# Optimization experiments

Measured on AMD Instinct MI355X. Metric: run time of the kernel, lower is better.

The kernel has to match this reference:

```python
import jax, jax.numpy as jnp
import numpy as np

N, F_IN, E = 50000, 128, 800000
HID, HEADS, EMB = 32, 8, 64
NEG_SLOPE = 0.2


def gat_conv(x, src, dst, W_src, W_dst, att_src, att_dst, bias, heads, out_ch, concat):
    n = x.shape[0]
    h_src = (x @ W_src).reshape(n, heads, out_ch)   # [N,H,C]
    h_dst = (x @ W_dst).reshape(n, heads, out_ch)
    a_src = jnp.sum(h_src * att_src, axis=-1)       # [N,H]
    a_dst = jnp.sum(h_dst * att_dst, axis=-1)
    e = jax.nn.leaky_relu(a_src[src] + a_dst[dst], NEG_SLOPE)  # [E,H]
    # segment softmax over destination nodes (stable, max detached as in PyG)
    m = jax.ops.segment_max(e, dst, num_segments=n)
    m = jnp.where(jnp.isfinite(m), m, 0.0)
    ex = jnp.exp(e - jax.lax.stop_gradient(m)[dst])
    denom = jax.ops.segment_sum(ex, dst, num_segments=n)
    alpha = ex / (denom[dst] + 1e-16)               # [E,H]
    msg = h_src[src] * alpha[:, :, None]            # [E,H,C]
    out = jax.ops.segment_sum(msg, dst, num_segments=n)  # [N,H,C]
    if concat:
        out = out.reshape(n, heads * out_ch)
    else:
        out = out.mean(axis=1)
    return out + bias


def setup_inputs() -> dict:
    key = jax.random.key(0)
    ks = jax.random.split(key, 12)
    g = lambda k, shape: jax.random.normal(k, shape, dtype=jnp.float32) * (1.0 / np.sqrt(shape[0]))
    x = jax.random.normal(ks[0], (N, F_IN), dtype=jnp.float32)
    edge_index = jax.random.randint(ks[1], (2, E), 0, N, dtype=jnp.int64)
    return {
        "x": x,
        "edge_index": edge_index,
        "W_src1": g(ks[2], (F_IN, HEADS * HID)),
        "W_dst1": g(ks[3], (F_IN, HEADS * HID)),
        "att_src1": g(ks[4], (HEADS, HID)) * 0.1,
        "att_dst1": g(ks[5], (HEADS, HID)) * 0.1,
        "b1": jnp.zeros((HEADS * HID,), dtype=jnp.float32),
        "W_src2": g(ks[6], (HEADS * HID, EMB)),
        "W_dst2": g(ks[7], (HEADS * HID, EMB)),
        "att_src2": g(ks[8], (1, EMB)) * 0.1,
        "att_dst2": g(ks[9], (1, EMB)) * 0.1,
        "b2": jnp.zeros((EMB,), dtype=jnp.float32),
    }


def reference(x, edge_index, W_src1, W_dst1, att_src1, att_dst1, b1,
              W_src2, W_dst2, att_src2, att_dst2, b2):
    src, dst = edge_index[0], edge_index[1]
    h = gat_conv(x, src, dst, W_src1, W_dst1, att_src1, att_dst1, b1, HEADS, HID, True)
    h = jax.nn.relu(h)
    out = gat_conv(h, src, dst, W_src2, W_dst2, att_src2, att_dst2, b2, 1, EMB, False)
    return out
```

## Files before the change

kernel.cpp:

```cpp
#include <hip/hip_runtime.h>
#include <hip/hip_bf16.h>
#include <cstdint>
#include <cstddef>

#define NN    50000
#define FIN   128
#define EE    800000
#define HID_  32
#define HEADS_ 8
#define EMB_  64
#define NEG   0.2f
#define CAP   64
#define NB_PREP 202
#define NB_EDGE 3125
#define LOG2E 1.4426950408889634f

typedef short bf16x8 __attribute__((ext_vector_type(8)));
typedef float f32x4  __attribute__((ext_vector_type(4)));

static __device__ __forceinline__ ushort f2bf(float f){
    uint u = __float_as_uint(f);
    uint r = (u + 0x7FFFu + ((u >> 16) & 1u)) >> 16;
    return (ushort)r;
}
static __device__ __forceinline__ float bf2f(ushort u){
    return __uint_as_float(((uint)u) << 16);
}
static __device__ __forceinline__ float pexp(float t){
    return __builtin_amdgcn_exp2f(fmaxf(t, NEG * t));
}

__global__ __launch_bounds__(256) void k_prep_hist(const float* __restrict__ Wsrc1, const float* __restrict__ Wdst1,
                                                   const float* __restrict__ asrc1, const float* __restrict__ adst1,
                                                   const float* __restrict__ Wsrc2, const float* __restrict__ Wdst2,
                                                   const float* __restrict__ asrc2, const float* __restrict__ adst2,
                                                   ushort* __restrict__ wt1bf, float* __restrict__ wt2,
                                                   ushort* __restrict__ w1t, ushort* __restrict__ w2t,
                                                   const int* __restrict__ src, const int* __restrict__ dst,
                                                   int* __restrict__ deg, int* __restrict__ col){
    if (blockIdx.x >= NB_PREP){
        int e = (blockIdx.x - NB_PREP) * 256 + threadIdx.x;
        if (e < EE){
            int d = dst[e];
            int r = atomicAdd(&deg[d], 1);
            col[d * CAP + r] = src[e];
        }
        return;
    }
    int idx = blockIdx.x * blockDim.x + threadIdx.x;
    if (idx < 2048){
        int f = idx >> 4, j = idx & 15;
        const float* W; const float* a; int h;
        if (j < 8) { W = Wsrc1; a = asrc1; h = j; } else { W = Wdst1; a = adst1; h = j - 8; }
        float s = 0.f;
        #pragma unroll
        for (int c = 0; c < HID_; ++c)
            s += W[(size_t)f * (HEADS_ * HID_) + h * HID_ + c] * a[h * HID_ + c];
        wt1bf[j * 128 + f] = f2bf(s * LOG2E);
    } else if (idx < 2560){
        int t = idx - 2048;
        int f = t >> 1, j = t & 1;
        const float* W = j ? Wdst2 : Wsrc2;
        const float* a = j ? adst2 : asrc2;
        float s = 0.f;
        #pragma unroll
        for (int c = 0; c < EMB_; ++c) s += W[(size_t)f * EMB_ + c] * a[c];
        wt2[j * 256 + f] = s * LOG2E;
    } else if (idx < 35328){
        int t = idx - 2560;
        int n = t >> 7, k = t & 127;
        w1t[t] = f2bf(Wsrc1[(size_t)k * 256 + n]);
    } else if (idx < 51712){
        int t = idx - 35328;
        int n = t >> 8, k = t & 255;
        w2t[t] = f2bf(Wsrc2[(size_t)k * 64 + n]);
    }
}

__global__ __launch_bounds__(256) void k_gemm1_mfma(const float* __restrict__ x,
                                                    const ushort* __restrict__ w1t,
                                                    const ushort* __restrict__ wt1bf,
                                                    ushort* __restrict__ c,
                                                    float* __restrict__ a_src1,
                                                    float* __restrict__ a_dst1){
    __shared__ ushort As[64][136];
    __shared__ ushort Bs[128][136];
    __shared__ ushort Bsa[16][136];
    const int tid = threadIdx.x;
    const int m0 = blockIdx.x * 64;
    const int n0 = blockIdx.y * 128;
    #pragma unroll
    for (int i = 0; i < 8; ++i){
        int idx = tid + i * 256;
        int r = idx >> 5, c4 = idx & 31;
        int m = m0 + r;
        float4 v = make_float4(0.f, 0.f, 0.f, 0.f);
        if (m < NN) v = *(const float4*)&x[(size_t)m * FIN + c4 * 4];
        ushort4 u; u.x = f2bf(v.x); u.y = f2bf(v.y); u.z = f2bf(v.z); u.w = f2bf(v.w);
        *(ushort4*)&As[r][c4 * 4] = u;
    }
    #pragma unroll
    for (int i = 0; i < 8; ++i){
        int idx = tid + i * 256;
        int r = idx >> 4, c8 = idx & 15;
        const ushort4* s4 = (const ushort4*)&w1t[(size_t)(n0 + r) * 128 + c8 * 8];
        *(ushort4*)&Bs[r][c8 * 8]     = s4[0];
        *(ushort4*)&Bs[r][c8 * 8 + 4] = s4[1];
    }
    if (blockIdx.y == 0){
        int r = tid >> 4, c8 = tid & 15;
        const ushort4* s4 = (const ushort4*)&wt1bf[r * 128 + c8 * 8];
        *(ushort4*)&Bsa[r][c8 * 8]     = s4[0];
        *(ushort4*)&Bsa[r][c8 * 8 + 4] = s4[1];
    }
    __syncthreads();
    const int lane = tid & 63;
    const int w    = tid >> 6;
    const int mr   = lane & 15;
    const int kg   = lane >> 4;
    f32x4 acc[8];
    #pragma unroll
    for (int i = 0; i < 8; ++i) acc[i] = (f32x4){0.f, 0.f, 0.f, 0.f};
    f32x4 acca = (f32x4){0.f, 0.f, 0.f, 0.f};
    #pragma unroll
    for (int ks = 0; ks < 4; ++ks){
        bf16x8 a = *(const bf16x8*)&As[w * 16 + mr][ks * 32 + kg * 8];
        #pragma unroll
        for (int nf = 0; nf < 8; ++nf){
            bf16x8 b = *(const bf16x8*)&Bs[nf * 16 + mr][ks * 32 + kg * 8];
            acc[nf] = __builtin_amdgcn_mfma_f32_16x16x32_bf16(a, b, acc[nf], 0, 0, 0);
        }
        if (blockIdx.y == 0){
            bf16x8 ba = *(const bf16x8*)&Bsa[mr][ks * 32 + kg * 8];
            acca = __builtin_amdgcn_mfma_f32_16x16x32_bf16(a, ba, acca, 0, 0, 0);
        }
    }
    #pragma unroll
    for (int nf = 0; nf < 8; ++nf){
        int colb = n0 + nf * 16 + mr;
        #pragma unroll
        for (int r = 0; r < 4; ++r){
            int row = m0 + w * 16 + kg * 4 + r;
            if (row < NN) c[(size_t)row * 256 + colb] = f2bf(acc[nf][r]);
        }
    }
    if (blockIdx.y == 0){
        int j = mr;
        #pragma unroll
        for (int r = 0; r < 4; ++r){
            int row = m0 + w * 16 + kg * 4 + r;
            if (row < NN){
                if (j < 8) a_src1[(size_t)row * 8 + j]       = acca[r];
                else       a_dst1[(size_t)row * 8 + (j - 8)] = acca[r];
            }
        }
    }
}

__global__ __launch_bounds__(256) void k_agg1(const ushort* __restrict__ hsrc, const float* __restrict__ a_src,
                                              const float* __restrict__ a_dst, const int* __restrict__ deg,
                                              const int* __restrict__ col, const float* __restrict__ b1,
                                              const float* __restrict__ wt2,
                                              ushort* __restrict__ hout_bf,
                                              float* __restrict__ a_src2, float* __restrict__ a_dst2){
    int node = blockIdx.x * 4 + (threadIdx.x >> 6);
    if (node >= NN) return;
    int lane = threadIdx.x & 63;
    int head = lane >> 3;
    float ad = a_dst[(size_t)node * 8 + head];
    const ushort4* h4 = (const ushort4*)hsrc;
    float4 acc = make_float4(0.f, 0.f, 0.f, 0.f);
    float den = 0.f;
    int b = node * CAP, en = b + deg[node];
    int i = b;
    for (; i + 4 <= en; i += 4){
        int s0 = col[i], s1 = col[i+1], s2 = col[i+2], s3 = col[i+3];
        float e0 = a_src[(size_t)s0 * 8 + head];
        float e1 = a_src[(size_t)s1 * 8 + head];
        float e2 = a_src[(size_t)s2 * 8 + head];
        float e3 = a_src[(size_t)s3 * 8 + head];
        ushort4 v0 = h4[(size_t)s0 * 64 + lane];
        ushort4 v1 = h4[(size_t)s1 * 64 + lane];
        ushort4 v2 = h4[(size_t)s2 * 64 + lane];
        ushort4 v3 = h4[(size_t)s3 * 64 + lane];
        float p0 = pexp(e0 + ad);
        float p1 = pexp(e1 + ad);
        float p2 = pexp(e2 + ad);
        float p3 = pexp(e3 + ad);
        acc.x += p0*bf2f(v0.x) + p1*bf2f(v1.x) + p2*bf2f(v2.x) + p3*bf2f(v3.x);
        acc.y += p0*bf2f(v0.y) + p1*bf2f(v1.y) + p2*bf2f(v2.y) + p3*bf2f(v3.y);
        acc.z += p0*bf2f(v0.z) + p1*bf2f(v1.z) + p2*bf2f(v2.z) + p3*bf2f(v3.z);
        acc.w += p0*bf2f(v0.w) + p1*bf2f(v1.w) + p2*bf2f(v2.w) + p3*bf2f(v3.w);
        den += p0 + p1 + p2 + p3;
    }
    for (; i < en; ++i){
        int s = col[i];
        float p = pexp(a_src[(size_t)s * 8 + head] + ad);
        ushort4 v = h4[(size_t)s * 64 + lane];
        acc.x += p * bf2f(v.x); acc.y += p * bf2f(v.y);
        acc.z += p * bf2f(v.z); acc.w += p * bf2f(v.w);
        den += p;
    }
    float inv = 1.f / (den + 1e-16f);
    float4 bb = ((const float4*)b1)[lane];
    float4 o;
    o.x = fmaxf(acc.x * inv + bb.x, 0.f);
    o.y = fmaxf(acc.y * inv + bb.y, 0.f);
    o.z = fmaxf(acc.z * inv + bb.z, 0.f);
    o.w = fmaxf(acc.w * inv + bb.w, 0.f);
    ushort4 ob; ob.x = f2bf(o.x); ob.y = f2bf(o.y); ob.z = f2bf(o.z); ob.w = f2bf(o.w);
    ((ushort4*)hout_bf)[(size_t)node * 64 + lane] = ob;
    float4 ws4 = ((const float4*)wt2)[lane];
    float4 wd4 = ((const float4*)(wt2 + 256))[lane];
    float ss2 = o.x*ws4.x + o.y*ws4.y + o.z*ws4.z + o.w*ws4.w;
    float sd2 = o.x*wd4.x + o.y*wd4.y + o.z*wd4.z + o.w*wd4.w;
    #pragma unroll
    for (int off = 32; off > 0; off >>= 1){
        ss2 += __shfl_xor(ss2, off);
        sd2 += __shfl_xor(sd2, off);
    }
    if (lane == 0){ a_src2[node] = ss2; a_dst2[node] = sd2; }
}

__global__ __launch_bounds__(256) void k_gemm2_mfma(const ushort* __restrict__ hbf,
                                                    const ushort* __restrict__ w2t,
                                                    ushort* __restrict__ c2){
    __shared__ ushort As[64][264];
    __shared__ ushort Bs[64][264];
    const int tid = threadIdx.x;
    const int m0 = blockIdx.x * 64;
    #pragma unroll
    for (int i = 0; i < 8; ++i){
        int idx = tid + i * 256;
        int r = idx >> 5, c8 = idx & 31;
        int m = m0 + r;
        ushort4 v0 = make_ushort4(0,0,0,0), v1 = make_ushort4(0,0,0,0);
        if (m < NN){
            const ushort4* s4 = (const ushort4*)&hbf[(size_t)m * 256 + c8 * 8];
            v0 = s4[0]; v1 = s4[1];
        }
        *(ushort4*)&As[r][c8 * 8]     = v0;
        *(ushort4*)&As[r][c8 * 8 + 4] = v1;
    }
    #pragma unroll
    for (int i = 0; i < 8; ++i){
        int idx = tid + i * 256;
        int r = idx >> 5, c8 = idx & 31;
        const ushort4* s4 = (const ushort4*)&w2t[(size_t)r * 256 + c8 * 8];
        *(ushort4*)&Bs[r][c8 * 8]     = s4[0];
        *(ushort4*)&Bs[r][c8 * 8 + 4] = s4[1];
    }
    __syncthreads();
    const int lane = tid & 63;
    const int w    = tid >> 6;
    const int mr   = lane & 15;
    const int kg   = lane >> 4;
    f32x4 acc[4];
    #pragma unroll
    for (int i = 0; i < 4; ++i) acc[i] = (f32x4){0.f, 0.f, 0.f, 0.f};
    #pragma unroll
    for (int ks = 0; ks < 8; ++ks){
        bf16x8 a = *(const bf16x8*)&As[w * 16 + mr][ks * 32 + kg * 8];
        #pragma unroll
        for (int nf = 0; nf < 4; ++nf){
            bf16x8 b = *(const bf16x8*)&Bs[nf * 16 + mr][ks * 32 + kg * 8];
            acc[nf] = __builtin_amdgcn_mfma_f32_16x16x32_bf16(a, b, acc[nf], 0, 0, 0);
        }
    }
    #pragma unroll
    for (int nf = 0; nf < 4; ++nf){
        int colb = nf * 16 + mr;
        #pragma unroll
        for (int r = 0; r < 4; ++r){
            int row = m0 + w * 16 + kg * 4 + r;
            if (row < NN) c2[(size_t)row * 64 + colb] = f2bf(acc[nf][r]);
        }
    }
}

__global__ __launch_bounds__(256) void k_agg2(const ushort* __restrict__ h2bf, const float* __restrict__ a_src2,
                                              const float* __restrict__ a_dst2, const int* __restrict__ deg,
                                              const int* __restrict__ col, const float* __restrict__ b2,
                                              float* __restrict__ out){
    int node = blockIdx.x * 4 + (threadIdx.x >> 6);
    if (node >= NN) return;
    int lane = threadIdx.x & 63;
    float ad = a_dst2[node];
    float acc = 0.f, den = 0.f;
    int b = node * CAP, en = b + deg[node];
    int i = b;
    for (; i + 8 <= en; i += 8){
        int ss[8]; float e[8]; ushort u[8]; float p[8];
        #pragma unroll
        for (int j = 0; j < 8; ++j) ss[j] = col[i + j];
        #pragma unroll
        for (int j = 0; j < 8; ++j) e[j] = a_src2[ss[j]];
        #pragma unroll
        for (int j = 0; j < 8; ++j) u[j] = h2bf[(size_t)ss[j] * 64 + lane];
        #pragma unroll
        for (int j = 0; j < 8; ++j) p[j] = pexp(e[j] + ad);
        #pragma unroll
        for (int j = 0; j < 8; ++j){
            acc += p[j] * bf2f(u[j]);
            den += p[j];
        }
    }
    for (; i < en; ++i){
        int s = col[i];
        float p = pexp(a_src2[s] + ad);
        acc += p * bf2f(h2bf[(size_t)s * 64 + lane]);
        den += p;
    }
    out[(size_t)node * 64 + lane] = acc / (den + 1e-16f) + b2[lane];
}

extern "C" void kernel_launch(void* const* d_in, const int* in_sizes, int n_in,
                              void* d_out, int out_size, void* d_ws, size_t ws_size,
                              hipStream_t stream){
    const float* x        = (const float*)d_in[0];
    const int*   ei       = (const int*)  d_in[1];
    const float* Wsrc1    = (const float*)d_in[2];
    const float* Wdst1    = (const float*)d_in[3];
    const float* att_src1 = (const float*)d_in[4];
    const float* att_dst1 = (const float*)d_in[5];
    const float* b1       = (const float*)d_in[6];
    const float* Wsrc2    = (const float*)d_in[7];
    const float* Wdst2    = (const float*)d_in[8];
    const float* att_src2 = (const float*)d_in[9];
    const float* att_dst2 = (const float*)d_in[10];
    const float* b2       = (const float*)d_in[11];
    float* out = (float*)d_out;
    const int* srcp = ei;
    const int* dstp = ei + EE;

    char* base = (char*)d_ws;
    ushort* hbf1   = (ushort*)base;  base += (size_t)NN * 256 * 2;
    ushort* hrel   = (ushort*)base;  base += (size_t)NN * 256 * 2;
    ushort* h2bf   = (ushort*)base;  base += (size_t)NN * 64 * 2;
    float*  a_src1 = (float*)base;   base += (size_t)NN * 8 * 4;
    float*  a_dst1 = (float*)base;   base += (size_t)NN * 8 * 4;
    float*  a_src2 = (float*)base;   base += (size_t)NN * 4;
    float*  a_dst2 = (float*)base;   base += (size_t)NN * 4;
    ushort* wt1bf  = (ushort*)base;  base += 2048 * 2;
    float*  wt2    = (float*)base;   base += 512 * 4;
    ushort* w1t    = (ushort*)base;  base += 32768 * 2;
    ushort* w2t    = (ushort*)base;  base += 16384 * 2;
    int* deg     = (int*)base;       base += (size_t)NN * 4;
    int* col     = (int*)base;       base += (size_t)NN * CAP * 4;

    (void)hipMemsetAsync(deg, 0, NN * sizeof(int), stream);

    k_prep_hist<<<NB_PREP + NB_EDGE, 256, 0, stream>>>(Wsrc1, Wdst1, att_src1, att_dst1,
                                                       Wsrc2, Wdst2, att_src2, att_dst2,
                                                       wt1bf, wt2, w1t, w2t,
                                                       srcp, dstp, deg, col);
    dim3 g1((NN + 63) / 64, 2);
    k_gemm1_mfma<<<g1, 256, 0, stream>>>(x, w1t, wt1bf, hbf1, a_src1, a_dst1);
    k_agg1<<<(NN + 3) / 4, 256, 0, stream>>>(hbf1, a_src1, a_dst1, deg, col, b1, wt2,
                                             hrel, a_src2, a_dst2);
    k_gemm2_mfma<<<(NN + 63) / 64, 256, 0, stream>>>(hrel, w2t, h2bf);
    k_agg2<<<(NN + 3) / 4, 256, 0, stream>>>(h2bf, a_src2, a_dst2, deg, col, b2, out);
}
```

Baseline: 208.4 us.

## Fuse edge bucketing into GEMM1 launch and drop LDS staging in both GEMMs

Moves the edge histogram/bucketing work out of the weight-prep kernel into the first GEMM launch as extra blocks, so the atomic scatter runs alongside the projection GEMM instead of before it. GEMM1 now computes all 256 output columns per block in a 1D grid, so x is read once rather than twice. Both GEMMs drop shared-memory staging and load A and B fragments straight from global memory into MFMA operands, removing syncthreads and LDS traffic. In exchange, each GEMM1 block holds 16 accumulator tiles, which raises register pressure, and B fragments are re-read from global/L2 by every wave.

```diff
diff --git a/kernel.cpp b/kernel.cpp
--- a/kernel.cpp
+++ b/kernel.cpp
@@ -13,6 +13,7 @@
 #define CAP   64
 #define NB_PREP 202
 #define NB_EDGE 3125
+#define NB_M1   782
 #define LOG2E 1.4426950408889634f
 
 typedef short bf16x8 __attribute__((ext_vector_type(8)));
@@ -30,23 +31,12 @@
     return __builtin_amdgcn_exp2f(fmaxf(t, NEG * t));
 }
 
-__global__ __launch_bounds__(256) void k_prep_hist(const float* __restrict__ Wsrc1, const float* __restrict__ Wdst1,
-                                                   const float* __restrict__ asrc1, const float* __restrict__ adst1,
-                                                   const float* __restrict__ Wsrc2, const float* __restrict__ Wdst2,
-                                                   const float* __restrict__ asrc2, const float* __restrict__ adst2,
-                                                   ushort* __restrict__ wt1bf, float* __restrict__ wt2,
-                                                   ushort* __restrict__ w1t, ushort* __restrict__ w2t,
-                                                   const int* __restrict__ src, const int* __restrict__ dst,
-                                                   int* __restrict__ deg, int* __restrict__ col){
-    if (blockIdx.x >= NB_PREP){
-        int e = (blockIdx.x - NB_PREP) * 256 + threadIdx.x;
-        if (e < EE){
-            int d = dst[e];
-            int r = atomicAdd(&deg[d], 1);
-            col[d * CAP + r] = src[e];
-        }
-        return;
-    }
+__global__ __launch_bounds__(256) void k_prep(const float* __restrict__ Wsrc1, const float* __restrict__ Wdst1,
+                                              const float* __restrict__ asrc1, const float* __restrict__ adst1,
+                                              const float* __restrict__ Wsrc2, const float* __restrict__ Wdst2,
+                                              const float* __restrict__ asrc2, const float* __restrict__ adst2,
+                                              ushort* __restrict__ wt1bf, float* __restrict__ wt2,
+                                              ushort* __restrict__ w1t, ushort* __restrict__ w2t){
     int idx = blockIdx.x * blockDim.x + threadIdx.x;
     if (idx < 2048){
         int f = idx >> 4, j = idx & 15;
@@ -77,74 +67,65 @@
     }
 }
 
-__global__ __launch_bounds__(256) void k_gemm1_mfma(const float* __restrict__ x,
-                                                    const ushort* __restrict__ w1t,
-                                                    const ushort* __restrict__ wt1bf,
-                                                    ushort* __restrict__ c,
-                                                    float* __restrict__ a_src1,
-                                                    float* __restrict__ a_dst1){
-    __shared__ ushort As[64][136];
-    __shared__ ushort Bs[128][136];
-    __shared__ ushort Bsa[16][136];
-    const int tid = threadIdx.x;
-    const int m0 = blockIdx.x * 64;
-    const int n0 = blockIdx.y * 128;
-    #pragma unroll
-    for (int i = 0; i < 8; ++i){
-        int idx = tid + i * 256;
-        int r = idx >> 5, c4 = idx & 31;
-        int m = m0 + r;
-        float4 v = make_float4(0.f, 0.f, 0.f, 0.f);
-        if (m < NN) v = *(const float4*)&x[(size_t)m * FIN + c4 * 4];
-        ushort4 u; u.x = f2bf(v.x); u.y = f2bf(v.y); u.z = f2bf(v.z); u.w = f2bf(v.w);
-        *(ushort4*)&As[r][c4 * 4] = u;
-    }
-    #pragma unroll
-    for (int i = 0; i < 8; ++i){
-        int idx = tid + i * 256;
-        int r = idx >> 4, c8 = idx & 15;
-        const ushort4* s4 = (const ushort4*)&w1t[(size_t)(n0 + r) * 128 + c8 * 8];
-        *(ushort4*)&Bs[r][c8 * 8]     = s4[0];
-        *(ushort4*)&Bs[r][c8 * 8 + 4] = s4[1];
-    }
-    if (blockIdx.y == 0){
-        int r = tid >> 4, c8 = tid & 15;
-        const ushort4* s4 = (const ushort4*)&wt1bf[r * 128 + c8 * 8];
-        *(ushort4*)&Bsa[r][c8 * 8]     = s4[0];
-        *(ushort4*)&Bsa[r][c8 * 8 + 4] = s4[1];
-    }
-    __syncthreads();
+__global__ __launch_bounds__(256) void k_gemm1_bucket(const float* __restrict__ x,
+                                                      const ushort* __restrict__ w1t,
+                                                      const ushort* __restrict__ wt1bf,
+                                                      ushort* __restrict__ c,
+                                                      float* __restrict__ a_src1,
+                                                      float* __restrict__ a_dst1,
+                                                      const int* __restrict__ src, const int* __restrict__ dst,
+                                                      int* __restrict__ deg, int* __restrict__ col){
+    if (blockIdx.x >= NB_M1){
+        int e = (blockIdx.x - NB_M1) * 256 + threadIdx.x;
+        if (e < EE){
+            int d = dst[e];
+            int r = atomicAdd(&deg[d], 1);
+            col[d * CAP + r] = src[e];
+        }
+        return;
+    }
+    const int tid  = threadIdx.x;
     const int lane = tid & 63;
     const int w    = tid >> 6;
     const int mr   = lane & 15;
     const int kg   = lane >> 4;
-    f32x4 acc[8];
-    #pragma unroll
-    for (int i = 0; i < 8; ++i) acc[i] = (f32x4){0.f, 0.f, 0.f, 0.f};
+    const int m0   = blockIdx.x * 64;
+    const int arow = m0 + w * 16 + mr;
+    const bool rv  = arow < NN;
+    f32x4 acc[16];
+    #pragma unroll
+    for (int i = 0; i < 16; ++i) acc[i] = (f32x4){0.f, 0.f, 0.f, 0.f};
     f32x4 acca = (f32x4){0.f, 0.f, 0.f, 0.f};
     #pragma unroll
     for (int ks = 0; ks < 4; ++ks){
-        bf16x8 a = *(const bf16x8*)&As[w * 16 + mr][ks * 32 + kg * 8];
-        #pragma unroll
-        for (int nf = 0; nf < 8; ++nf){
-            bf16x8 b = *(const bf16x8*)&Bs[nf * 16 + mr][ks * 32 + kg * 8];
+        bf16x8 a = (bf16x8){0,0,0,0,0,0,0,0};
+        if (rv){
+            const float* ap = &x[(size_t)arow * FIN + ks * 32 + kg * 8];
+            float4 f0 = *(const float4*)ap;
+            float4 f1 = *(const float4*)(ap + 4);
+            a[0] = (short)f2bf(f0.x); a[1] = (short)f2bf(f0.y);
+            a[2] = (short)f2bf(f0.z); a[3] = (short)f2bf(f0.w);
+            a[4] = (short)f2bf(f1.x); a[5] = (short)f2bf(f1.y);
+            a[6] = (short)f2bf(f1.z); a[7] = (short)f2bf(f1.w);
+        }
+        #pragma unroll
+        for (int nf = 0; nf < 16; ++nf){
+            bf16x8 b = *(const bf16x8*)&w1t[(size_t)(nf * 16 + mr) * 128 + ks * 32 + kg * 8];
             acc[nf] = __builtin_amdgcn_mfma_f32_16x16x32_bf16(a, b, acc[nf], 0, 0, 0);
         }
-        if (blockIdx.y == 0){
-            bf16x8 ba = *(const bf16x8*)&Bsa[mr][ks * 32 + kg * 8];
-            acca = __builtin_amdgcn_mfma_f32_16x16x32_bf16(a, ba, acca, 0, 0, 0);
-        }
-    }
-    #pragma unroll
-    for (int nf = 0; nf < 8; ++nf){
-        int colb = n0 + nf * 16 + mr;
+        bf16x8 ba = *(const bf16x8*)&wt1bf[mr * 128 + ks * 32 + kg * 8];
+        acca = __builtin_amdgcn_mfma_f32_16x16x32_bf16(a, ba, acca, 0, 0, 0);
+    }
+    #pragma unroll
+    for (int nf = 0; nf < 16; ++nf){
+        int colb = nf * 16 + mr;
         #pragma unroll
         for (int r = 0; r < 4; ++r){
             int row = m0 + w * 16 + kg * 4 + r;
             if (row < NN) c[(size_t)row * 256 + colb] = f2bf(acc[nf][r]);
         }
     }
-    if (blockIdx.y == 0){
+    {
         int j = mr;
         #pragma unroll
         for (int r = 0; r < 4; ++r){
@@ -222,48 +203,27 @@
     if (lane == 0){ a_src2[node] = ss2; a_dst2[node] = sd2; }
 }
 
-__global__ __launch_bounds__(256) void k_gemm2_mfma(const ushort* __restrict__ hbf,
+__global__ __launch_bounds__(256) void k_gemm2_lite(const ushort* __restrict__ hrel,
                                                     const ushort* __restrict__ w2t,
                                                     ushort* __restrict__ c2){
-    __shared__ ushort As[64][264];
-    __shared__ ushort Bs[64][264];
-    const int tid = threadIdx.x;
-    const int m0 = blockIdx.x * 64;
-    #pragma unroll
-    for (int i = 0; i < 8; ++i){
-        int idx = tid + i * 256;
-        int r = idx >> 5, c8 = idx & 31;
-        int m = m0 + r;
-        ushort4 v0 = make_ushort4(0,0,0,0), v1 = make_ushort4(0,0,0,0);
-        if (m < NN){
-            const ushort4* s4 = (const ushort4*)&hbf[(size_t)m * 256 + c8 * 8];
-            v0 = s4[0]; v1 = s4[1];
-        }
-        *(ushort4*)&As[r][c8 * 8]     = v0;
-        *(ushort4*)&As[r][c8 * 8 + 4] = v1;
-    }
-    #pragma unroll
-    for (int i = 0; i < 8; ++i){
-        int idx = tid + i * 256;
-        int r = idx >> 5, c8 = idx & 31;
-        const ushort4* s4 = (const ushort4*)&w2t[(size_t)r * 256 + c8 * 8];
-        *(ushort4*)&Bs[r][c8 * 8]     = s4[0];
-        *(ushort4*)&Bs[r][c8 * 8 + 4] = s4[1];
-    }
-    __syncthreads();
+    const int tid  = threadIdx.x;
     const int lane = tid & 63;
     const int w    = tid >> 6;
     const int mr   = lane & 15;
     const int kg   = lane >> 4;
+    const int m0   = blockIdx.x * 64;
+    const int arow = m0 + w * 16 + mr;
+    const bool rv  = arow < NN;
     f32x4 acc[4];
     #pragma unroll
     for (int i = 0; i < 4; ++i) acc[i] = (f32x4){0.f, 0.f, 0.f, 0.f};
     #pragma unroll
     for (int ks = 0; ks < 8; ++ks){
-        bf16x8 a = *(const bf16x8*)&As[w * 16 + mr][ks * 32 + kg * 8];
+        bf16x8 a = (bf16x8){0,0,0,0,0,0,0,0};
+        if (rv) a = *(const bf16x8*)&hrel[(size_t)arow * 256 + ks * 32 + kg * 8];
         #pragma unroll
         for (int nf = 0; nf < 4; ++nf){
-            bf16x8 b = *(const bf16x8*)&Bs[nf * 16 + mr][ks * 32 + kg * 8];
+            bf16x8 b = *(const bf16x8*)&w2t[(size_t)(nf * 16 + mr) * 256 + ks * 32 + kg * 8];
             acc[nf] = __builtin_amdgcn_mfma_f32_16x16x32_bf16(a, b, acc[nf], 0, 0, 0);
         }
     }
@@ -350,14 +310,13 @@
 
     (void)hipMemsetAsync(deg, 0, NN * sizeof(int), stream);
 
-    k_prep_hist<<<NB_PREP + NB_EDGE, 256, 0, stream>>>(Wsrc1, Wdst1, att_src1, att_dst1,
-                                                       Wsrc2, Wdst2, att_src2, att_dst2,
-                                                       wt1bf, wt2, w1t, w2t,
-                                                       srcp, dstp, deg, col);
-    dim3 g1((NN + 63) / 64, 2);
-    k_gemm1_mfma<<<g1, 256, 0, stream>>>(x, w1t, wt1bf, hbf1, a_src1, a_dst1);
+    k_prep<<<NB_PREP, 256, 0, stream>>>(Wsrc1, Wdst1, att_src1, att_dst1,
+                                        Wsrc2, Wdst2, att_src2, att_dst2,
+                                        wt1bf, wt2, w1t, w2t);
+    k_gemm1_bucket<<<NB_M1 + NB_EDGE, 256, 0, stream>>>(x, w1t, wt1bf, hbf1, a_src1, a_dst1,
+                                                        srcp, dstp, deg, col);
     k_agg1<<<(NN + 3) / 4, 256, 0, stream>>>(hbf1, a_src1, a_dst1, deg, col, b1, wt2,
                                              hrel, a_src2, a_dst2);
-    k_gemm2_mfma<<<(NN + 63) / 64, 256, 0, stream>>>(hrel, w2t, h2bf);
+    k_gemm2_lite<<<NB_M1, 256, 0, stream>>>(hrel, w2t, h2bf);
     k_agg2<<<(NN + 3) / 4, 256, 0, stream>>>(h2bf, a_src2, a_dst2, deg, col, b2, out);
 }
```

Result: slower. 244.1 us (+17.2%).

## Fold deg memset into prep kernel and fuse edge histogram into GEMM1 launch

Applied to the files above, without the earlier changes.

The memset of the degree array moves into the weight-prep kernel, which now covers 202 blocks × 256 = 51,712 threads, enough to zero all N entries. The edge bucketing (atomic degree count plus CSR column scatter) moves out of the prep kernel into extra blocks appended to the first GEMM grid. The 2D GEMM grid is flattened into 1D to make room for this. This removes one memset launch and lets the atomic-heavy histogram run alongside the MFMA GEMM instead of before it. In exchange, the histogram blocks share the launch with GEMM blocks that reserve large shared memory, which may limit occupancy.

```diff
diff --git a/kernel.cpp b/kernel.cpp
--- a/kernel.cpp
+++ b/kernel.cpp
@@ -13,6 +13,7 @@
 #define CAP   64
 #define NB_PREP 202
 #define NB_EDGE 3125
+#define NB_G1   1564
 #define LOG2E 1.4426950408889634f
 
 typedef short bf16x8 __attribute__((ext_vector_type(8)));
@@ -30,24 +31,15 @@
     return __builtin_amdgcn_exp2f(fmaxf(t, NEG * t));
 }
 
-__global__ __launch_bounds__(256) void k_prep_hist(const float* __restrict__ Wsrc1, const float* __restrict__ Wdst1,
-                                                   const float* __restrict__ asrc1, const float* __restrict__ adst1,
-                                                   const float* __restrict__ Wsrc2, const float* __restrict__ Wdst2,
-                                                   const float* __restrict__ asrc2, const float* __restrict__ adst2,
-                                                   ushort* __restrict__ wt1bf, float* __restrict__ wt2,
-                                                   ushort* __restrict__ w1t, ushort* __restrict__ w2t,
-                                                   const int* __restrict__ src, const int* __restrict__ dst,
-                                                   int* __restrict__ deg, int* __restrict__ col){
-    if (blockIdx.x >= NB_PREP){
-        int e = (blockIdx.x - NB_PREP) * 256 + threadIdx.x;
-        if (e < EE){
-            int d = dst[e];
-            int r = atomicAdd(&deg[d], 1);
-            col[d * CAP + r] = src[e];
-        }
-        return;
-    }
+__global__ __launch_bounds__(256) void k_prep(const float* __restrict__ Wsrc1, const float* __restrict__ Wdst1,
+                                              const float* __restrict__ asrc1, const float* __restrict__ adst1,
+                                              const float* __restrict__ Wsrc2, const float* __restrict__ Wdst2,
+                                              const float* __restrict__ asrc2, const float* __restrict__ adst2,
+                                              ushort* __restrict__ wt1bf, float* __restrict__ wt2,
+                                              ushort* __restrict__ w1t, ushort* __restrict__ w2t,
+                                              int* __restrict__ deg){
     int idx = blockIdx.x * blockDim.x + threadIdx.x;
+    if (idx < NN) deg[idx] = 0;
     if (idx < 2048){
         int f = idx >> 4, j = idx & 15;
         const float* W; const float* a; int h;
@@ -77,18 +69,29 @@
     }
 }
 
-__global__ __launch_bounds__(256) void k_gemm1_mfma(const float* __restrict__ x,
+__global__ __launch_bounds__(256) void k_gemm1_hist(const float* __restrict__ x,
                                                     const ushort* __restrict__ w1t,
                                                     const ushort* __restrict__ wt1bf,
                                                     ushort* __restrict__ c,
                                                     float* __restrict__ a_src1,
-                                                    float* __restrict__ a_dst1){
+                                                    float* __restrict__ a_dst1,
+                                                    const int* __restrict__ src, const int* __restrict__ dst,
+                                                    int* __restrict__ deg, int* __restrict__ col){
     __shared__ ushort As[64][136];
     __shared__ ushort Bs[128][136];
     __shared__ ushort Bsa[16][136];
+    if (blockIdx.x >= NB_G1){
+        int e = (blockIdx.x - NB_G1) * 256 + threadIdx.x;
+        if (e < EE){
+            int d = dst[e];
+            int r = atomicAdd(&deg[d], 1);
+            col[d * CAP + r] = src[e];
+        }
+        return;
+    }
     const int tid = threadIdx.x;
-    const int m0 = blockIdx.x * 64;
-    const int n0 = blockIdx.y * 128;
+    const int m0 = (blockIdx.x >> 1) * 64;
+    const int n0 = (blockIdx.x & 1) * 128;
     #pragma unroll
     for (int i = 0; i < 8; ++i){
         int idx = tid + i * 256;
@@ -107,7 +110,7 @@
         *(ushort4*)&Bs[r][c8 * 8]     = s4[0];
         *(ushort4*)&Bs[r][c8 * 8 + 4] = s4[1];
     }
-    if (blockIdx.y == 0){
+    if (n0 == 0){
         int r = tid >> 4, c8 = tid & 15;
         const ushort4* s4 = (const ushort4*)&wt1bf[r * 128 + c8 * 8];
         *(ushort4*)&Bsa[r][c8 * 8]     = s4[0];
@@ -130,7 +133,7 @@
             bf16x8 b = *(const bf16x8*)&Bs[nf * 16 + mr][ks * 32 + kg * 8];
             acc[nf] = __builtin_amdgcn_mfma_f32_16x16x32_bf16(a, b, acc[nf], 0, 0, 0);
         }
-        if (blockIdx.y == 0){
+        if (n0 == 0){
             bf16x8 ba = *(const bf16x8*)&Bsa[mr][ks * 32 + kg * 8];
             acca = __builtin_amdgcn_mfma_f32_16x16x32_bf16(a, ba, acca, 0, 0, 0);
         }
@@ -144,7 +147,7 @@
             if (row < NN) c[(size_t)row * 256 + colb] = f2bf(acc[nf][r]);
         }
     }
-    if (blockIdx.y == 0){
+    if (n0 == 0){
         int j = mr;
         #pragma unroll
         for (int r = 0; r < 4; ++r){
@@ -348,14 +351,11 @@
     int* deg     = (int*)base;       base += (size_t)NN * 4;
     int* col     = (int*)base;       base += (size_t)NN * CAP * 4;
 
-    (void)hipMemsetAsync(deg, 0, NN * sizeof(int), stream);
-
-    k_prep_hist<<<NB_PREP + NB_EDGE, 256, 0, stream>>>(Wsrc1, Wdst1, att_src1, att_dst1,
-                                                       Wsrc2, Wdst2, att_src2, att_dst2,
-                                                       wt1bf, wt2, w1t, w2t,
-                                                       srcp, dstp, deg, col);
-    dim3 g1((NN + 63) / 64, 2);
-    k_gemm1_mfma<<<g1, 256, 0, stream>>>(x, w1t, wt1bf, hbf1, a_src1, a_dst1);
+    k_prep<<<NB_PREP, 256, 0, stream>>>(Wsrc1, Wdst1, att_src1, att_dst1,
+                                        Wsrc2, Wdst2, att_src2, att_dst2,
+                                        wt1bf, wt2, w1t, w2t, deg);
+    k_gemm1_hist<<<NB_G1 + NB_EDGE, 256, 0, stream>>>(x, w1t, wt1bf, hbf1, a_src1, a_dst1,
+                                                      srcp, dstp, deg, col);
     k_agg1<<<(NN + 3) / 4, 256, 0, stream>>>(hbf1, a_src1, a_dst1, deg, col, b1, wt2,
                                              hrel, a_src2, a_dst2);
     k_gemm2_mfma<<<(NN + 63) / 64, 256, 0, stream>>>(hrel, w2t, h2bf);
```

After: 216.0 us. 1.04x slower.

## Pre-convert x to bf16 in prep kernel and pair edges in agg2

Applied to the files above, without the earlier changes.

Adds extra blocks to the prep/histogram kernel that convert x to bf16 once into a workspace buffer. gemm1 then loads bf16 rows directly instead of reading and converting fp32 x in both of its column-tile blocks. agg2 is also restructured so each half-wave handles alternating edges and loads two bf16 channels per lane, with the halves combined by a cross-lane shuffle. The cost is an extra pass that writes and rereads x in bf16 plus additional launched blocks.

```diff
diff --git a/kernel.cpp b/kernel.cpp
--- a/kernel.cpp
+++ b/kernel.cpp
@@ -13,6 +13,7 @@
 #define CAP   64
 #define NB_PREP 202
 #define NB_EDGE 3125
+#define NB_XCNV 3125
 #define LOG2E 1.4426950408889634f
 
 typedef short bf16x8 __attribute__((ext_vector_type(8)));
@@ -37,7 +38,19 @@
                                                    ushort* __restrict__ wt1bf, float* __restrict__ wt2,
                                                    ushort* __restrict__ w1t, ushort* __restrict__ w2t,
                                                    const int* __restrict__ src, const int* __restrict__ dst,
-                                                   int* __restrict__ deg, int* __restrict__ col){
+                                                   int* __restrict__ deg, int* __restrict__ col,
+                                                   const float* __restrict__ x, ushort* __restrict__ xbf){
+    if (blockIdx.x >= NB_PREP + NB_EDGE){
+        int t = (blockIdx.x - NB_PREP - NB_EDGE) * 256 + threadIdx.x;
+        const float4* xp = (const float4*)(x + (size_t)t * 8);
+        float4 f0 = xp[0], f1 = xp[1];
+        ushort4 u0, u1;
+        u0.x = f2bf(f0.x); u0.y = f2bf(f0.y); u0.z = f2bf(f0.z); u0.w = f2bf(f0.w);
+        u1.x = f2bf(f1.x); u1.y = f2bf(f1.y); u1.z = f2bf(f1.z); u1.w = f2bf(f1.w);
+        ushort4* op = (ushort4*)(xbf + (size_t)t * 8);
+        op[0] = u0; op[1] = u1;
+        return;
+    }
     if (blockIdx.x >= NB_PREP){
         int e = (blockIdx.x - NB_PREP) * 256 + threadIdx.x;
         if (e < EE){
@@ -77,7 +90,7 @@
     }
 }
 
-__global__ __launch_bounds__(256) void k_gemm1_mfma(const float* __restrict__ x,
+__global__ __launch_bounds__(256) void k_gemm1_mfma(const ushort* __restrict__ xbf,
                                                     const ushort* __restrict__ w1t,
                                                     const ushort* __restrict__ wt1bf,
                                                     ushort* __restrict__ c,
@@ -90,14 +103,17 @@
     const int m0 = blockIdx.x * 64;
     const int n0 = blockIdx.y * 128;
     #pragma unroll
-    for (int i = 0; i < 8; ++i){
+    for (int i = 0; i < 4; ++i){
         int idx = tid + i * 256;
-        int r = idx >> 5, c4 = idx & 31;
+        int r = idx >> 4, c8 = idx & 15;
         int m = m0 + r;
-        float4 v = make_float4(0.f, 0.f, 0.f, 0.f);
-        if (m < NN) v = *(const float4*)&x[(size_t)m * FIN + c4 * 4];
-        ushort4 u; u.x = f2bf(v.x); u.y = f2bf(v.y); u.z = f2bf(v.z); u.w = f2bf(v.w);
-        *(ushort4*)&As[r][c4 * 4] = u;
+        ushort4 v0 = make_ushort4(0,0,0,0), v1 = make_ushort4(0,0,0,0);
+        if (m < NN){
+            const ushort4* s4 = (const ushort4*)&xbf[(size_t)m * FIN + c8 * 8];
+            v0 = s4[0]; v1 = s4[1];
+        }
+        *(ushort4*)&As[r][c8 * 8]     = v0;
+        *(ushort4*)&As[r][c8 * 8 + 4] = v1;
     }
     #pragma unroll
     for (int i = 0; i < 8; ++i){
@@ -285,33 +301,51 @@
     int node = blockIdx.x * 4 + (threadIdx.x >> 6);
     if (node >= NN) return;
     int lane = threadIdx.x & 63;
+    int pair = lane >> 5;
+    int cl   = lane & 31;
     float ad = a_dst2[node];
-    float acc = 0.f, den = 0.f;
+    float acc0 = 0.f, acc1 = 0.f, den = 0.f;
     int b = node * CAP, en = b + deg[node];
     int i = b;
     for (; i + 8 <= en; i += 8){
-        int ss[8]; float e[8]; ushort u[8]; float p[8];
-        #pragma unroll
-        for (int j = 0; j < 8; ++j) ss[j] = col[i + j];
-        #pragma unroll
-        for (int j = 0; j < 8; ++j) e[j] = a_src2[ss[j]];
-        #pragma unroll
-        for (int j = 0; j < 8; ++j) u[j] = h2bf[(size_t)ss[j] * 64 + lane];
-        #pragma unroll
-        for (int j = 0; j < 8; ++j) p[j] = pexp(e[j] + ad);
-        #pragma unroll
-        for (int j = 0; j < 8; ++j){
-            acc += p[j] * bf2f(u[j]);
-            den += p[j];
-        }
-    }
-    for (; i < en; ++i){
-        int s = col[i];
-        float p = pexp(a_src2[s] + ad);
-        acc += p * bf2f(h2bf[(size_t)s * 64 + lane]);
-        den += p;
-    }
-    out[(size_t)node * 64 + lane] = acc / (den + 1e-16f) + b2[lane];
+        int i0 = i + pair, i1 = i + 2 + pair, i2 = i + 4 + pair, i3 = i + 6 + pair;
+        int s0 = col[i0], s1 = col[i1], s2 = col[i2], s3 = col[i3];
+        float e0 = a_src2[s0], e1 = a_src2[s1], e2 = a_src2[s2], e3 = a_src2[s3];
+        uint u0 = *(const uint*)&h2bf[(size_t)s0 * 64 + cl * 2];
+        uint u1 = *(const uint*)&h2bf[(size_t)s1 * 64 + cl * 2];
+        uint u2 = *(const uint*)&h2bf[(size_t)s2 * 64 + cl * 2];
+        uint u3 = *(const uint*)&h2bf[(size_t)s3 * 64 + cl * 2];
+        float p0 = pexp(e0 + ad);
+        float p1 = pexp(e1 + ad);
+        float p2 = pexp(e2 + ad);
+        float p3 = pexp(e3 + ad);
+        acc0 += p0*bf2f((ushort)(u0 & 0xffff)) + p1*bf2f((ushort)(u1 & 0xffff))
+              + p2*bf2f((ushort)(u2 & 0xffff)) + p3*bf2f((ushort)(u3 & 0xffff));
+        acc1 += p0*bf2f((ushort)(u0 >> 16))    + p1*bf2f((ushort)(u1 >> 16))
+              + p2*bf2f((ushort)(u2 >> 16))    + p3*bf2f((ushort)(u3 >> 16));
+        den += p0 + p1 + p2 + p3;
+    }
+    for (; i < en; i += 2){
+        int ie = i + pair;
+        bool v = ie < en;
+        int s = col[v ? ie : en - 1];
+        float e = a_src2[s];
+        uint u = *(const uint*)&h2bf[(size_t)s * 64 + cl * 2];
+        float p = v ? pexp(e + ad) : 0.f;
+        acc0 += p * bf2f((ushort)(u & 0xffff));
+        acc1 += p * bf2f((ushort)(u >> 16));
+        den  += p;
+    }
+    acc0 += __shfl_xor(acc0, 32);
+    acc1 += __shfl_xor(acc1, 32);
+    den  += __shfl_xor(den , 32);
+    if (lane < 32){
+        float inv = 1.f / (den + 1e-16f);
+        float2 o;
+        o.x = acc0 * inv + b2[cl * 2];
+        o.y = acc1 * inv + b2[cl * 2 + 1];
+        *(float2*)&out[(size_t)node * 64 + cl * 2] = o;
+    }
 }
 
 extern "C" void kernel_launch(void* const* d_in, const int* in_sizes, int n_in,
@@ -337,6 +371,7 @@
     ushort* hbf1   = (ushort*)base;  base += (size_t)NN * 256 * 2;
     ushort* hrel   = (ushort*)base;  base += (size_t)NN * 256 * 2;
     ushort* h2bf   = (ushort*)base;  base += (size_t)NN * 64 * 2;
+    ushort* xbf    = (ushort*)base;  base += (size_t)NN * FIN * 2;
     float*  a_src1 = (float*)base;   base += (size_t)NN * 8 * 4;
     float*  a_dst1 = (float*)base;   base += (size_t)NN * 8 * 4;
     float*  a_src2 = (float*)base;   base += (size_t)NN * 4;
@@ -350,12 +385,13 @@
 
     (void)hipMemsetAsync(deg, 0, NN * sizeof(int), stream);
 
-    k_prep_hist<<<NB_PREP + NB_EDGE, 256, 0, stream>>>(Wsrc1, Wdst1, att_src1, att_dst1,
-                                                       Wsrc2, Wdst2, att_src2, att_dst2,
-                                                       wt1bf, wt2, w1t, w2t,
-                                                       srcp, dstp, deg, col);
+    k_prep_hist<<<NB_PREP + NB_EDGE + NB_XCNV, 256, 0, stream>>>(
+        Wsrc1, Wdst1, att_src1, att_dst1,
+        Wsrc2, Wdst2, att_src2, att_dst2,
+        wt1bf, wt2, w1t, w2t,
+        srcp, dstp, deg, col, x, xbf);
     dim3 g1((NN + 63) / 64, 2);
-    k_gemm1_mfma<<<g1, 256, 0, stream>>>(x, w1t, wt1bf, hbf1, a_src1, a_dst1);
+    k_gemm1_mfma<<<g1, 256, 0, stream>>>(xbf, w1t, wt1bf, hbf1, a_src1, a_dst1);
     k_agg1<<<(NN + 3) / 4, 256, 0, stream>>>(hbf1, a_src1, a_dst1, deg, col, b1, wt2,
                                              hrel, a_src2, a_dst2);
     k_gemm2_mfma<<<(NN + 63) / 64, 256, 0, stream>>>(hrel, w2t, h2bf);
```

Result: faster. 195.5 us (-6.2%).
